# Kernel tuning notes

Measured on AMD Instinct MI355X. Metric: run time of the kernel, lower is better.

The kernel has to match this reference:

```python
import jax, jax.numpy as jnp
import numpy as np

DEGREE = 3
NUM_KNOTS_PARAM = 5
NUM_BASIS = NUM_KNOTS_PARAM + DEGREE - 1  # 7


def bspline_basis(x, knots, degree=DEGREE, nb=NUM_BASIS):
    """Faithful vectorization of BSplineBasis.compute_basis.

    x: [B, D]; knots: [num_knots] strictly increasing (linspace -> all
    denominator != 0 and i+d+1 < num_knots checks in the torch code are
    statically true). Returns [B, D, nb].
    """
    x = jnp.clip(x, knots[0], knots[-1])
    xe = x[..., None]  # [B, D, 1]
    # degree-0: indicator over first nb knot intervals (as in the torch loop)
    b = ((xe >= knots[:nb]) & (xe < knots[1 : nb + 1])).astype(x.dtype)
    for d in range(1, degree + 1):
        left = (xe - knots[:nb]) / (knots[d : d + nb] - knots[:nb])
        right = (knots[d + 1 : d + 1 + nb] - xe) / (
            knots[d + 1 : d + 1 + nb] - knots[1 : 1 + nb]
        )
        # torch code drops basis[:, :, i+1] when i+1 == nb -> shifted with zero pad
        b_shift = jnp.pad(b[..., 1:], ((0, 0), (0, 0), (0, 1)))
        b = left * b + right * b_shift
    return b


def setup_inputs() -> dict:
    key = jax.random.key(0)
    k1, k2, k3, k4 = jax.random.split(key, 4)
    B, IN, OUT = 8192, 1024, 1024
    x = jax.random.normal(k1, (B, IN), dtype=jnp.float32)
    spline_weights = 0.1 * jax.random.normal(k2, (IN, OUT, NUM_BASIS), dtype=jnp.float32)
    bound = 1.0 / np.sqrt(IN)
    W = jax.random.uniform(k3, (OUT, IN), minval=-bound, maxval=bound, dtype=jnp.float32)
    b = jax.random.uniform(k4, (OUT,), minval=-bound, maxval=bound, dtype=jnp.float32)
    knots = jnp.linspace(-1.0, 1.0, NUM_KNOTS_PARAM + 2 * DEGREE, dtype=jnp.float32)
    return {"x": x, "spline_weights": spline_weights, "W": W, "b": b, "knots": knots}


def reference(x, spline_weights, W, b, knots):
    basis = bspline_basis(jnp.tanh(x), knots)  # [B, IN, NB]
    spline_out = jnp.einsum("bik,iok->bo", basis, spline_weights)
    linear_out = x @ W.T + b
    return linear_out + spline_out
```

## Files before the change

### kernel.cpp

```cpp
#include <hip/hip_runtime.h>
#include <cstdint>
#include <cstddef>

#define IN_DIM  1024
#define OUT_DIM 1024
#define NB      7
#define KTOT    8192
#define BROWS   8192

typedef unsigned short u16;
typedef __attribute__((ext_vector_type(8))) short bf16x8;
typedef __attribute__((ext_vector_type(8))) unsigned short u16x8;
typedef __attribute__((ext_vector_type(4))) float f32x4;

__device__ __forceinline__ u16 f2bf(float f) {
    union { float f; unsigned int u; } v; v.f = f;
    unsigned int r = (v.u + 0x7fffu + ((v.u >> 16) & 1u)) >> 16;
    return (u16)r;
}

__device__ __forceinline__ void gl_lds16(const u16* g, u16* l) {
    __builtin_amdgcn_global_load_lds(
        (const __attribute__((address_space(1))) void*)g,
        (__attribute__((address_space(3))) void*)l,
        16, 0, 0);
}

__global__ __launch_bounds__(256) void prep_wsw(const float* __restrict__ sw,
                                                const float* __restrict__ W,
                                                u16* __restrict__ Bt) {
    __shared__ u16 S[8 * 256 * 8];
    const int i0 = blockIdx.x * 8;
    const int o0 = blockIdx.y * 256;
    const int t  = threadIdx.x;
    #pragma unroll
    for (int il = 0; il < 8; ++il) {
        const float* src = sw + ((size_t)(i0 + il) * OUT_DIM + o0) * NB;
        for (int c = t; c < 256 * NB; c += 256) {
            int ol = c / 7, k = c - ol * 7;
            S[(il * 256 + ol) * 8 + 1 + k] = f2bf(src[c]);
        }
    }
    for (int c = t; c < 2048; c += 256) {
        int ol = c >> 3, il = c & 7;
        S[(il * 256 + ol) * 8] = f2bf(W[(size_t)(o0 + ol) * IN_DIM + i0 + il]);
    }
    __syncthreads();
    for (int c = t; c < 2048; c += 256) {
        int ol = c >> 3, il = c & 7;
        *(u16x8*)&Bt[(size_t)(o0 + ol) * KTOT + (size_t)(i0 + il) * 8] =
            *(const u16x8*)&S[(il * 256 + ol) * 8];
    }
}

__global__ __launch_bounds__(256) void prep_a(const float* __restrict__ x,
                                              u16* __restrict__ A, int row0) {
    int gid = blockIdx.x * 256 + threadIdx.x;
    int b = gid >> 10;
    int i = gid & 1023;
    float xv = x[(size_t)(row0 + b) * IN_DIM + i];

    float e = __expf(2.f * xv);
    float t = 1.f - 2.f / (e + 1.f);
    t = fminf(fmaxf(t, -1.f), 1.f);

    const float kn[11] = {-1.f, -0.8f, -0.6f, -0.4f, -0.2f, 0.f,
                           0.2f, 0.4f, 0.6f, 0.8f, 1.f};
    float bb[8];
    #pragma unroll
    for (int j = 0; j < 7; ++j)
        bb[j] = (t >= kn[j] && t < kn[j + 1]) ? 1.f : 0.f;
    bb[7] = 0.f;

    const float rcp[4] = {0.f, 5.f, 2.5f, 5.f / 3.f};
    #pragma unroll
    for (int d = 1; d <= 3; ++d) {
        #pragma unroll
        for (int j = 0; j < 7; ++j) {
            float left  = (t - kn[j]) * rcp[d];
            float right = (kn[j + d + 1] - t) * rcp[d];
            bb[j] = left * bb[j] + right * bb[j + 1];
        }
    }
    u16x8 outv;
    outv[0] = f2bf(xv);
    #pragma unroll
    for (int k = 0; k < NB; ++k) outv[1 + k] = f2bf(bb[k]);
    *(u16x8*)&A[(size_t)b * KTOT + (size_t)i * 8] = outv;
}

__global__ __launch_bounds__(256) void gemm_bt(const u16* __restrict__ A,
                                               const u16* __restrict__ Bt,
                                               const float* __restrict__ bias,
                                               float* __restrict__ C) {
    __shared__ __align__(16) u16 As[128 * 128];
    __shared__ __align__(16) u16 Bs[128 * 128];
    const int t = threadIdx.x;
    const int L = t & 63;
    const int w = t >> 6;
    const int wm = w & 1, wn = w >> 1;

    const int Lid = blockIdx.x;
    const int n_t = (Lid >> 3) & 7;
    const int m_t = (Lid & 7) + 8 * (Lid >> 6);
    const int m0 = m_t * 128;
    const int n0 = n_t * 128;

    f32x4 acc[4][4] = {};

    const int trow = t >> 4;
    const int qsw  = (t & 15) ^ trow;
    const u16* gA[8]; const u16* gB[8];
    u16* lA[8]; u16* lB[8];
    #pragma unroll
    for (int g = 0; g < 8; ++g) {
        gA[g] = A  + (size_t)(m0 + 16 * g + trow) * KTOT + qsw * 8;
        gB[g] = Bt + (size_t)(n0 + 16 * g + trow) * KTOT + qsw * 8;
        lA[g] = &As[(256 * g + t) * 8];
        lB[g] = &Bs[(256 * g + t) * 8];
    }

    const int lm  = L & 15;
    const int qd  = L >> 4;

    for (int ko = 0; ko < KTOT; ko += 128) {
        __syncthreads();
        #pragma unroll
        for (int g = 0; g < 8; ++g) gl_lds16(gA[g] + ko, lA[g]);
        #pragma unroll
        for (int g = 0; g < 8; ++g) gl_lds16(gB[g] + ko, lB[g]);
        __syncthreads();

        #pragma unroll
        for (int ks = 0; ks < 4; ++ks) {
            const int pq = ((ks * 4 + qd) ^ lm) * 8;
            bf16x8 af[4], bfr[4];
            #pragma unroll
            for (int mi = 0; mi < 4; ++mi)
                af[mi] = *(const bf16x8*)&As[(wm * 64 + mi * 16 + lm) * 128 + pq];
            #pragma unroll
            for (int ni = 0; ni < 4; ++ni)
                bfr[ni] = *(const bf16x8*)&Bs[(wn * 64 + ni * 16 + lm) * 128 + pq];
            #pragma unroll
            for (int mi = 0; mi < 4; ++mi)
                #pragma unroll
                for (int ni = 0; ni < 4; ++ni)
                    acc[mi][ni] = __builtin_amdgcn_mfma_f32_16x16x32_bf16(
                        af[mi], bfr[ni], acc[mi][ni], 0, 0, 0);
        }
    }

    const int r0 = qd * 4;
    #pragma unroll
    for (int ni = 0; ni < 4; ++ni) {
        int col = n0 + wn * 64 + ni * 16 + lm;
        float bv = bias[col];
        #pragma unroll
        for (int mi = 0; mi < 4; ++mi) {
            int rb = m0 + wm * 64 + mi * 16 + r0;
            f32x4 v = acc[mi][ni];
            #pragma unroll
            for (int rr = 0; rr < 4; ++rr)
                C[(size_t)(rb + rr) * OUT_DIM + col] = v[rr] + bv;
        }
    }
}

extern "C" void kernel_launch(void* const* d_in, const int* in_sizes, int n_in,
                              void* d_out, int out_size, void* d_ws, size_t ws_size,
                              hipStream_t stream) {
    (void)in_sizes; (void)n_in; (void)out_size;
    const float* x    = (const float*)d_in[0];
    const float* sw   = (const float*)d_in[1];
    const float* W    = (const float*)d_in[2];
    const float* bias = (const float*)d_in[3];
    float* out = (float*)d_out;

    const size_t btBytes = (size_t)OUT_DIM * KTOT * 2;
    u16* Bt = (u16*)d_ws;
    u16* A  = (u16*)((char*)d_ws + btBytes);

    prep_wsw<<<dim3(IN_DIM / 8, OUT_DIM / 256), 256, 0, stream>>>(sw, W, Bt);

    int nchunks = 1;
    if (ws_size < btBytes + (size_t)BROWS * KTOT * 2)       nchunks = 2;
    if (ws_size < btBytes + (size_t)(BROWS / 2) * KTOT * 2) nchunks = 4;
    if (ws_size < btBytes + (size_t)(BROWS / 4) * KTOT * 2) nchunks = 8;
    const int rows = BROWS / nchunks;

    for (int c = 0; c < nchunks; ++c) {
        int row0 = c * rows;
        prep_a<<<rows * 4, 256, 0, stream>>>(x, A, row0);
        gemm_bt<<<dim3(8 * (rows / 128)), 256, 0, stream>>>(
            A, Bt, bias, out + (size_t)row0 * OUT_DIM);
    }
}
```

Measured before the change: 283.2 us.

## Double-buffer GEMM LDS tiles with K=64 stages to overlap loads and MFMA

Result: no change. 279.8 us (-1.2%).

```diff
diff --git a/kernel.cpp b/kernel.cpp
--- a/kernel.cpp
+++ b/kernel.cpp
@@ -93,8 +93,8 @@
                                                const u16* __restrict__ Bt,
                                                const float* __restrict__ bias,
                                                float* __restrict__ C) {
-    __shared__ __align__(16) u16 As[128 * 128];
-    __shared__ __align__(16) u16 Bs[128 * 128];
+    __shared__ __align__(16) u16 As[2][128 * 64];
+    __shared__ __align__(16) u16 Bs[2][128 * 64];
     const int t = threadIdx.x;
     const int L = t & 63;
     const int w = t >> 6;
@@ -108,39 +108,49 @@
 
     f32x4 acc[4][4] = {};
 
-    const int trow = t >> 4;
-    const int qsw  = (t & 15) ^ trow;
-    const u16* gA[8]; const u16* gB[8];
-    u16* lA[8]; u16* lB[8];
-    #pragma unroll
-    for (int g = 0; g < 8; ++g) {
-        gA[g] = A  + (size_t)(m0 + 16 * g + trow) * KTOT + qsw * 8;
-        gB[g] = Bt + (size_t)(n0 + 16 * g + trow) * KTOT + qsw * 8;
-        lA[g] = &As[(256 * g + t) * 8];
-        lB[g] = &Bs[(256 * g + t) * 8];
+    const int trow = t >> 3;
+    const int qsw  = (t & 7) ^ (trow & 7);
+    const u16* gA[4]; const u16* gB[4];
+    int off[4];
+    #pragma unroll
+    for (int g = 0; g < 4; ++g) {
+        gA[g] = A  + (size_t)(m0 + 32 * g + trow) * KTOT + qsw * 8;
+        gB[g] = Bt + (size_t)(n0 + 32 * g + trow) * KTOT + qsw * 8;
+        off[g] = (256 * g + t) * 8;
     }
 
     const int lm  = L & 15;
     const int qd  = L >> 4;
 
-    for (int ko = 0; ko < KTOT; ko += 128) {
-        __syncthreads();
+    u16* pA  = &As[0][0];
+    u16* pAn = &As[1][0];
+    u16* pB  = &Bs[0][0];
+    u16* pBn = &Bs[1][0];
+
+    #pragma unroll
+    for (int g = 0; g < 4; ++g) gl_lds16(gA[g], pA + off[g]);
+    #pragma unroll
+    for (int g = 0; g < 4; ++g) gl_lds16(gB[g], pB + off[g]);
+    __syncthreads();
+
+    for (int ko = 0; ko < KTOT; ko += 64) {
+        if (ko + 64 < KTOT) {
+            #pragma unroll
+            for (int g = 0; g < 4; ++g) gl_lds16(gA[g] + ko + 64, pAn + off[g]);
+            #pragma unroll
+            for (int g = 0; g < 4; ++g) gl_lds16(gB[g] + ko + 64, pBn + off[g]);
+        }
+
         #pragma unroll
-        for (int g = 0; g < 8; ++g) gl_lds16(gA[g] + ko, lA[g]);
-        #pragma unroll
-        for (int g = 0; g < 8; ++g) gl_lds16(gB[g] + ko, lB[g]);
-        __syncthreads();
-
-        #pragma unroll
-        for (int ks = 0; ks < 4; ++ks) {
-            const int pq = ((ks * 4 + qd) ^ lm) * 8;
+        for (int ks = 0; ks < 2; ++ks) {
+            const int pq = ((ks * 4 + qd) ^ (lm & 7)) * 8;
             bf16x8 af[4], bfr[4];
             #pragma unroll
             for (int mi = 0; mi < 4; ++mi)
-                af[mi] = *(const bf16x8*)&As[(wm * 64 + mi * 16 + lm) * 128 + pq];
+                af[mi] = *(const bf16x8*)&pA[(wm * 64 + mi * 16 + lm) * 64 + pq];
             #pragma unroll
             for (int ni = 0; ni < 4; ++ni)
-                bfr[ni] = *(const bf16x8*)&Bs[(wn * 64 + ni * 16 + lm) * 128 + pq];
+                bfr[ni] = *(const bf16x8*)&pB[(wn * 64 + ni * 16 + lm) * 64 + pq];
             #pragma unroll
             for (int mi = 0; mi < 4; ++mi)
                 #pragma unroll
@@ -148,6 +158,11 @@
                     acc[mi][ni] = __builtin_amdgcn_mfma_f32_16x16x32_bf16(
                         af[mi], bfr[ni], acc[mi][ni], 0, 0, 0);
         }
+
+        __syncthreads();
+        u16* tmp;
+        tmp = pA; pA = pAn; pAn = tmp;
+        tmp = pB; pB = pBn; pBn = tmp;
     }
 
     const int r0 = qd * 4;
```
